# Optimization experiments

Hardware: AMD Instinct MI355X
Metric: run time of the kernel (lower is better)

## Reference

```python
import jax, jax.numpy as jnp
import numpy as np

DEPTH = 3  # message passing depth; loop runs DEPTH-1 times
N_ATOMS = 50000
N_BONDS = 100000
MAX_NB = 6
ATOM_FDIM = 133
BOND_FDIM = 147
HIDDEN = 512
N_MOLS = 128


def setup_inputs() -> dict:
    key = jax.random.key(0)
    ks = jax.random.split(key, 16)
    inp = {
        'f_atoms': jax.random.normal(ks[0], (N_ATOMS, ATOM_FDIM), jnp.float32),
        'f_bonds': jax.random.normal(ks[1], (N_BONDS, BOND_FDIM), jnp.float32),
        'ano_f_atoms': jax.random.normal(ks[2], (N_ATOMS, ATOM_FDIM), jnp.float32),
        'ano_f_bonds': jax.random.normal(ks[3], (N_BONDS, BOND_FDIM), jnp.float32),
        'Wi': jax.random.normal(ks[4], (HIDDEN, BOND_FDIM), jnp.float32) * 0.05,
        'Wh': jax.random.normal(ks[5], (HIDDEN, HIDDEN), jnp.float32) * 0.05,
        'Wo': jax.random.normal(ks[6], (HIDDEN, ATOM_FDIM + HIDDEN), jnp.float32) * 0.05,
        'bo': jax.random.normal(ks[7], (HIDDEN,), jnp.float32) * 0.05,
        'a2b': jax.random.randint(ks[8], (N_ATOMS, MAX_NB), 0, N_BONDS, jnp.int32),
        'b2a': jax.random.randint(ks[9], (N_BONDS,), 0, N_ATOMS, jnp.int32),
        'b2revb': jax.random.randint(ks[10], (N_BONDS,), 0, N_BONDS, jnp.int32),
        'mol_ids': jnp.sort(jax.random.randint(ks[11], (N_ATOMS,), 0, N_MOLS, jnp.int32)),
        'ano_a2b': jax.random.randint(ks[12], (N_ATOMS, MAX_NB), 0, N_BONDS, jnp.int32),
        'ano_b2a': jax.random.randint(ks[13], (N_BONDS,), 0, N_ATOMS, jnp.int32),
        'ano_b2revb': jax.random.randint(ks[14], (N_BONDS,), 0, N_BONDS, jnp.int32),
        'ano_mol_ids': jnp.sort(jax.random.randint(ks[15], (N_ATOMS,), 0, N_MOLS, jnp.int32)),
        'n_mols': N_MOLS,
    }
    return inp


def _encode(f_atoms, f_bonds, Wi, Wh, Wo, bo, a2b, b2a, b2revb, mol_ids, n_mols):
    # input = W_i(f_bonds); message = act(input)   [n_bonds, hidden]
    inp = f_bonds @ Wi.T
    message = jax.nn.relu(inp)
    for _ in range(DEPTH - 1):
        # gather neighbor bond messages per atom and sum: [n_atoms, max_nb, H] -> [n_atoms, H]
        a_message = message[a2b].sum(axis=1)
        # directed message update: incoming sum minus reverse bond message
        message = a_message[b2a] - message[b2revb]
        message = jax.nn.relu(inp + message @ Wh.T)
        # dropout p=0 -> identity
    # final atom readout
    a_message = message[a2b].sum(axis=1)                       # [n_atoms, H]
    a_input = jnp.concatenate([f_atoms, a_message], axis=1)    # [n_atoms, atom_fdim+H]
    atom_hiddens = jax.nn.relu(a_input @ Wo.T + bo)            # [n_atoms, H]
    # per-molecule mean pool (a_scope loop -> segment mean; empty mols -> zero vector)
    sums = jax.ops.segment_sum(atom_hiddens, mol_ids, num_segments=n_mols)
    counts = jax.ops.segment_sum(jnp.ones((atom_hiddens.shape[0],), atom_hiddens.dtype),
                                 mol_ids, num_segments=n_mols)
    return sums / jnp.maximum(counts, 1.0)[:, None]


def reference(f_atoms, f_bonds, ano_f_atoms, ano_f_bonds, Wi, Wh, Wo, bo,
              a2b, b2a, b2revb, mol_ids, ano_a2b, ano_b2a, ano_b2revb, ano_mol_ids, n_mols):
    mol_vecs = _encode(f_atoms, f_bonds, Wi, Wh, Wo, bo, a2b, b2a, b2revb, mol_ids, n_mols)
    ano_mol_vecs = _encode(ano_f_atoms, ano_f_bonds, Wi, Wh, Wo, bo,
                           ano_a2b, ano_b2a, ano_b2revb, ano_mol_ids, n_mols)
    return mol_vecs, ano_mol_vecs
```

## Files before the change

### kernel.cpp

```cpp
#include <hip/hip_runtime.h>

#define NAT 50000
#define NBND 100000
#define MAXNB 6
#define AF 133
#define BF 147
#define HID 512
#define NMOL 128
#define KP 672
#define MOFF 160

typedef __attribute__((ext_vector_type(8))) unsigned short us8;
typedef __attribute__((ext_vector_type(8))) short bfrag;
typedef __attribute__((ext_vector_type(4))) float f4;

__device__ __forceinline__ unsigned short f2bf(float f) {
    unsigned int x = __float_as_uint(f);
    unsigned int r = x + 0x7fffu + ((x >> 16) & 1u);
    return (unsigned short)(r >> 16);
}
__device__ __forceinline__ float bf2f(unsigned short u) {
    return __uint_as_float(((unsigned int)u) << 16);
}

__device__ __forceinline__ void dma16(const void* g, void* l) {
    __builtin_amdgcn_global_load_lds(
        (__attribute__((address_space(1))) void*)(void*)g,
        (__attribute__((address_space(3))) void*)l, 16, 0, 0);
}

__global__ void prep_catW(const float* __restrict__ Wi, const float* __restrict__ Wh,
                          unsigned short* __restrict__ catW) {
    int idx = blockIdx.x * 256 + threadIdx.x;
    if (idx >= HID * KP) return;
    int n = idx / KP, k = idx - n * KP;
    float v = 0.f;
    if (k < BF) v = Wi[n * BF + k];
    else if (k >= MOFF) v = Wh[n * HID + (k - MOFF)];
    catW[idx] = f2bf(v);
}
__global__ void prep_woW(const float* __restrict__ Wo, unsigned short* __restrict__ woW) {
    int idx = blockIdx.x * 256 + threadIdx.x;
    if (idx >= HID * KP) return;
    int n = idx / KP, k = idx - n * KP;
    float v = 0.f;
    if (k < AF) v = Wo[n * (AF + HID) + k];
    else if (k >= MOFF) v = Wo[n * (AF + HID) + (k - 27)];
    woW[idx] = f2bf(v);
}

template<int MODE>
__global__ __launch_bounds__(256) void gemm_mfma(
    const float* __restrict__ Afeat,
    const unsigned short* __restrict__ Amsg,
    const unsigned short* __restrict__ BW,
    const float* __restrict__ bias,
    unsigned short* __restrict__ outB,
    float* __restrict__ outF,
    int M)
{
    constexpr int FEAT  = (MODE == 2) ? AF : BF;
    constexpr int NK    = (MODE == 0) ? 5 : 21;
    constexpr int NFEAT = 5;

    __shared__ unsigned short As[2][128 * 32];
    __shared__ unsigned short Bs[2][128 * 32];

    int nwg = gridDim.x;
    int q = nwg >> 3, r = nwg & 7;
    int xcd = blockIdx.x & 7, pos = blockIdx.x >> 3;
    int newid = (xcd < r ? xcd * (q + 1) : r * (q + 1) + (xcd - r) * q) + pos;
    const int m0 = (newid >> 2) * 128;
    const int n0 = (newid & 3) * 128;

    const int tid  = threadIdx.x;
    const int lane = tid & 63;
    const int wid  = tid >> 6;
    const int wm   = wid >> 1;
    const int wn   = wid & 1;
    const int l15  = lane & 15;
    const int lg   = lane >> 4;

    const int drow = lane >> 2;
    const int dchk = lane & 3;
    const int slr   = tid >> 1;
    const int shalf = tid & 1;

    auto stageB = [&](int ks, int buf) {
#pragma unroll
        for (int j = 0; j < 2; j++) {
            int R0 = wid * 32 + j * 16;
            int lr = R0 + drow;
            int sw = (lr ^ (lr >> 2)) & 3;
            const unsigned short* src =
                BW + (size_t)(n0 + lr) * KP + ks * 32 + ((dchk ^ sw) << 3);
            dma16(src, &Bs[buf][R0 * 32]);
        }
    };
    auto stageA_dma = [&](int ks, int buf) {
        const int kb = ks * 32 - MOFF;
#pragma unroll
        for (int j = 0; j < 2; j++) {
            int R0 = wid * 32 + j * 16;
            int lr = R0 + drow;
            int gr = m0 + lr; gr = gr < M ? gr : M - 1;
            int sw = (lr ^ (lr >> 2)) & 3;
            const unsigned short* src =
                Amsg + (size_t)gr * HID + kb + ((dchk ^ sw) << 3);
            dma16(src, &As[buf][R0 * 32]);
        }
    };
    auto stageA_slow = [&](int ks, int buf) {
        const int k0 = ks * 32;
        const int gr = m0 + slr;
        const int sw = (slr ^ (slr >> 2)) & 3;
#pragma unroll
        for (int h = 0; h < 2; h++) {
            int c = shalf * 2 + h;
            us8 v = {0, 0, 0, 0, 0, 0, 0, 0};
            if (gr < M) {
#pragma unroll
                for (int e = 0; e < 8; e++) {
                    int k = k0 + c * 8 + e;
                    if (k < FEAT) v[e] = f2bf(Afeat[(size_t)gr * FEAT + k]);
                }
            }
            *(us8*)&As[buf][slr * 32 + ((c ^ sw) << 3)] = v;
        }
    };

    const f4 fzero = {0.f, 0.f, 0.f, 0.f};
    f4 acc[4][4];
#pragma unroll
    for (int i = 0; i < 4; i++)
#pragma unroll
        for (int j = 0; j < 4; j++) acc[i][j] = fzero;

    stageB(0, 0);
    stageA_slow(0, 0);
    __syncthreads();

    int cur = 0;
    for (int ks = 0; ks < NK; ks++) {
        const int nxt = ks + 1;
        const bool hn = nxt < NK;
        const bool fast = hn && (nxt >= NFEAT);
        if (hn) {
            stageB(nxt, cur ^ 1);
            if (fast) stageA_dma(nxt, cur ^ 1);
        }
        bfrag a[4], b[4];
#pragma unroll
        for (int mf = 0; mf < 4; mf++) {
            int rr = wm * 64 + mf * 16 + l15;
            int p = lg ^ ((rr ^ (rr >> 2)) & 3);
            a[mf] = *(const bfrag*)&As[cur][rr * 32 + p * 8];
        }
#pragma unroll
        for (int nf = 0; nf < 4; nf++) {
            int rr = wn * 64 + nf * 16 + l15;
            int p = lg ^ ((rr ^ (rr >> 2)) & 3);
            b[nf] = *(const bfrag*)&Bs[cur][rr * 32 + p * 8];
        }
#pragma unroll
        for (int mf = 0; mf < 4; mf++)
#pragma unroll
            for (int nf = 0; nf < 4; nf++)
                acc[mf][nf] = __builtin_amdgcn_mfma_f32_16x16x32_bf16(
                    a[mf], b[nf], acc[mf][nf], 0, 0, 0);
        __syncthreads();
        if (hn && !fast) {
            stageA_slow(nxt, cur ^ 1);
            __syncthreads();
        }
        cur ^= 1;
    }

#pragma unroll
    for (int mf = 0; mf < 4; mf++) {
#pragma unroll
        for (int rg = 0; rg < 4; rg++) {
            int R = m0 + wm * 64 + mf * 16 + lg * 4 + rg;
            if (R >= M) continue;
#pragma unroll
            for (int nf = 0; nf < 4; nf++) {
                int C = n0 + wn * 64 + nf * 16 + l15;
                float v = acc[mf][nf][rg];
                if (MODE == 2) {
                    v += bias[C];
                    outF[(size_t)R * HID + C] = fmaxf(v, 0.f);
                } else {
                    outB[(size_t)R * HID + C] = f2bf(fmaxf(v, 0.f));
                }
            }
        }
    }
}

__global__ void dm_k(const unsigned short* __restrict__ amsg,
                     const unsigned short* __restrict__ msg,
                     const int* __restrict__ b2a, const int* __restrict__ b2revb,
                     unsigned short* __restrict__ dm) {
    int t = blockIdx.x * 256 + threadIdx.x;
    if (t >= NBND * 64) return;
    int b = t >> 6, c8 = (t & 63) * 8;
    int ia = b2a[b], ir = b2revb[b];
    us8 x = *(const us8*)(amsg + (size_t)ia * HID + c8);
    us8 y = *(const us8*)(msg + (size_t)ir * HID + c8);
    us8 o;
#pragma unroll
    for (int j = 0; j < 8; j++) o[j] = f2bf(bf2f(x[j]) - bf2f(y[j]));
    *(us8*)(dm + (size_t)b * HID + c8) = o;
}

__global__ void gather_sum_k(const unsigned short* __restrict__ msg,
                             const int* __restrict__ a2b,
                             unsigned short* __restrict__ amsg) {
    int t = blockIdx.x * 256 + threadIdx.x;
    if (t >= NAT * 64) return;
    int a = t >> 6, c8 = (t & 63) * 8;
    float s[8];
#pragma unroll
    for (int j = 0; j < 8; j++) s[j] = 0.f;
#pragma unroll
    for (int nb = 0; nb < MAXNB; nb++) {
        int b = a2b[a * MAXNB + nb];
        us8 v = *(const us8*)(msg + (size_t)b * HID + c8);
#pragma unroll
        for (int j = 0; j < 8; j++) s[j] += bf2f(v[j]);
    }
    us8 o;
#pragma unroll
    for (int j = 0; j < 8; j++) o[j] = f2bf(s[j]);
    *(us8*)(amsg + (size_t)a * HID + c8) = o;
}

__global__ void pool_k(const float* __restrict__ ah, const int* __restrict__ mol_ids,
                       float* __restrict__ out) {
    int m = blockIdx.x;
    int c = blockIdx.y * 256 + threadIdx.x;
    int lo = 0, hi = NAT;
    while (lo < hi) { int mid = (lo + hi) >> 1; if (mol_ids[mid] < m) lo = mid + 1; else hi = mid; }
    int start = lo;
    hi = NAT;
    while (lo < hi) { int mid = (lo + hi) >> 1; if (mol_ids[mid] < m + 1) lo = mid + 1; else hi = mid; }
    int end = lo;
    float s = 0.f;
    for (int a = start; a < end; a++) s += ah[(size_t)a * HID + c];
    float cnt = (float)(end - start);
    out[(size_t)m * HID + c] = s / fmaxf(cnt, 1.f);
}

extern "C" void kernel_launch(void* const* d_in, const int* in_sizes, int n_in,
                              void* d_out, int out_size, void* d_ws, size_t ws_size,
                              hipStream_t stream) {
    const float* f_atoms     = (const float*)d_in[0];
    const float* f_bonds     = (const float*)d_in[1];
    const float* ano_f_atoms = (const float*)d_in[2];
    const float* ano_f_bonds = (const float*)d_in[3];
    const float* Wi = (const float*)d_in[4];
    const float* Wh = (const float*)d_in[5];
    const float* Wo = (const float*)d_in[6];
    const float* bo = (const float*)d_in[7];
    const int* a2b     = (const int*)d_in[8];
    const int* b2a     = (const int*)d_in[9];
    const int* b2revb  = (const int*)d_in[10];
    const int* mol_ids = (const int*)d_in[11];
    const int* ano_a2b     = (const int*)d_in[12];
    const int* ano_b2a     = (const int*)d_in[13];
    const int* ano_b2revb  = (const int*)d_in[14];
    const int* ano_mol_ids = (const int*)d_in[15];
    float* out = (float*)d_out;

    char* ws = (char*)d_ws;
    unsigned short* msgA = (unsigned short*)ws;  ws += (size_t)NBND * HID * 2;
    char* msgB_raw = ws;
    unsigned short* msgB = (unsigned short*)ws;  ws += (size_t)NBND * HID * 2;
    unsigned short* amsg = (unsigned short*)ws;  ws += (size_t)NAT * HID * 2;
    unsigned short* catW = (unsigned short*)ws;  ws += (size_t)HID * KP * 2;
    unsigned short* woW  = (unsigned short*)ws;  ws += (size_t)HID * KP * 2;

    const size_t need = ((size_t)2 * NBND + NAT) * HID * 2 + (size_t)2 * HID * KP * 2;
    if (ws_size < need) return;

    prep_catW<<<(HID * KP + 255) / 256, 256, 0, stream>>>(Wi, Wh, catW);
    prep_woW<<<(HID * KP + 255) / 256, 256, 0, stream>>>(Wo, woW);

    const int nwgB = 4 * ((NBND + 127) / 128);
    const int nwgA = 4 * ((NAT + 127) / 128);
    const int gsBlocks = (NAT * 64 + 255) / 256;
    const int dmBlocks = (NBND * 64 + 255) / 256;

    for (int e = 0; e < 2; e++) {
        const float* fa = e ? ano_f_atoms : f_atoms;
        const float* fb = e ? ano_f_bonds : f_bonds;
        const int* e_a2b = e ? ano_a2b : a2b;
        const int* e_b2a = e ? ano_b2a : b2a;
        const int* e_b2revb = e ? ano_b2revb : b2revb;
        const int* e_mids = e ? ano_mol_ids : mol_ids;

        gemm_mfma<0><<<nwgB, 256, 0, stream>>>(fb, (const unsigned short*)nullptr, catW,
                                               nullptr, msgA, nullptr, NBND);
        for (int d = 0; d < 2; d++) {
            gather_sum_k<<<gsBlocks, 256, 0, stream>>>(msgA, e_a2b, amsg);
            dm_k<<<dmBlocks, 256, 0, stream>>>(amsg, msgA, e_b2a, e_b2revb, msgB);
            gemm_mfma<1><<<nwgB, 256, 0, stream>>>(fb, msgB, catW,
                                                   nullptr, msgA, nullptr, NBND);
        }
        gather_sum_k<<<gsBlocks, 256, 0, stream>>>(msgA, e_a2b, amsg);
        float* ah = (float*)msgB_raw;
        gemm_mfma<2><<<nwgA, 256, 0, stream>>>(fa, amsg, woW,
                                               bo, nullptr, ah, NAT);
        pool_k<<<dim3(NMOL, 2), 256, 0, stream>>>(ah, e_mids, out + (size_t)e * NMOL * HID);
    }
}
```

Before: 1.971 ms.

## Triple-buffer GEMM LDS stages with prefetch distance two and vmcnt waits

Moves the MFMA GEMM from double to triple buffering in LDS, prefetching the tile two k-steps ahead. Full __syncthreads are replaced by explicit s_waitcnt vmcnt counts plus a raw s_barrier, so one step's loads can stay in flight while the current tile is computed. The slow path that converts features to bf16 is now issued ahead too, and the k-loop is fully unrolled. In exchange, LDS use grows by half, which can lower occupancy. The hand-counted vmcnt values must match the loads stageB/stageA actually issue, or a data race follows.

```diff
diff --git a/kernel.cpp b/kernel.cpp
--- a/kernel.cpp
+++ b/kernel.cpp
@@ -28,6 +28,8 @@
         (__attribute__((address_space(1))) void*)(void*)g,
         (__attribute__((address_space(3))) void*)l, 16, 0, 0);
 }
+
+#define WAITVM(N) asm volatile("s_waitcnt vmcnt(" #N ")" ::: "memory")
 
 __global__ void prep_catW(const float* __restrict__ Wi, const float* __restrict__ Wh,
                           unsigned short* __restrict__ catW) {
@@ -63,8 +65,8 @@
     constexpr int NK    = (MODE == 0) ? 5 : 21;
     constexpr int NFEAT = 5;
 
-    __shared__ unsigned short As[2][128 * 32];
-    __shared__ unsigned short Bs[2][128 * 32];
+    __shared__ unsigned short As[3][128 * 32];
+    __shared__ unsigned short Bs[3][128 * 32];
 
     int nwg = gridDim.x;
     int q = nwg >> 3, r = nwg & 7;
@@ -136,18 +138,19 @@
 #pragma unroll
         for (int j = 0; j < 4; j++) acc[i][j] = fzero;
 
-    stageB(0, 0);
-    stageA_slow(0, 0);
+    stageB(0, 0); stageA_slow(0, 0);
+    if (NK > 1) { stageB(1, 1); stageA_slow(1, 1); }
     __syncthreads();
 
-    int cur = 0;
+#pragma unroll
     for (int ks = 0; ks < NK; ks++) {
-        const int nxt = ks + 1;
-        const bool hn = nxt < NK;
-        const bool fast = hn && (nxt >= NFEAT);
-        if (hn) {
-            stageB(nxt, cur ^ 1);
-            if (fast) stageA_dma(nxt, cur ^ 1);
+        const int cur = ks % 3;
+        const int nx2 = ks + 2;
+        if (nx2 < NK) {
+            const int pb = nx2 % 3;
+            stageB(nx2, pb);
+            if (nx2 >= NFEAT) stageA_dma(nx2, pb);
+            else              stageA_slow(nx2, pb);
         }
         bfrag a[4], b[4];
 #pragma unroll
@@ -168,12 +171,16 @@
             for (int nf = 0; nf < 4; nf++)
                 acc[mf][nf] = __builtin_amdgcn_mfma_f32_16x16x32_bf16(
                     a[mf], b[nf], acc[mf][nf], 0, 0, 0);
-        __syncthreads();
-        if (hn && !fast) {
-            stageA_slow(nxt, cur ^ 1);
-            __syncthreads();
-        }
-        cur ^= 1;
+        if (ks < NK - 1) {
+            if (nx2 < NK) {
+                if (nx2 >= NFEAT) WAITVM(4);
+                else              WAITVM(2);
+            } else {
+                WAITVM(0);
+            }
+            __builtin_amdgcn_s_barrier();
+            __builtin_amdgcn_sched_barrier(0);
+        }
     }
 
 #pragma unroll
```

Result: faster. 1.883 ms (-4.5%).
